# Performance work log

Measured on AMD Instinct MI355X. Metric: run time of the kernel, lower is better.

The kernel has to match this reference:

```python
import jax, jax.numpy as jnp
import numpy as np

N, E, ND, ED, NG = 100000, 1600000, 256, 32, 64
H1, H2 = 5, 1  # hard-coded hidden widths in the module
EPS = 1e-5


def setup_inputs() -> dict:
    key = jax.random.key(0)
    ks = jax.random.split(key, 32)

    def rn(k, shape, scale=0.05):
        return jax.random.normal(k, shape, dtype=jnp.float32) * scale

    inp = {
        "x": rn(ks[0], (N, ND), 1.0),
        "edge_attr": rn(ks[1], (E, ED), 1.0),
        "edge_index": jax.random.randint(ks[2], (2, E), 0, N, dtype=jnp.int32),
        "batch_idx": jnp.sort(jax.random.randint(ks[3], (N,), 0, NG, dtype=jnp.int32)),
        # conv1: ResGatedGraphConv(ND -> H1) with edge_dim=ED, root_weight, bias
        "Wk1": rn(ks[4], (ND, H1)), "bk1": jnp.zeros((H1,), jnp.float32),
        "Wq1": rn(ks[5], (ND, H1)), "bq1": jnp.zeros((H1,), jnp.float32),
        "Wv1": rn(ks[6], (ND, H1)), "bv1": jnp.zeros((H1,), jnp.float32),
        "We1": rn(ks[7], (ED, H1)), "be1": jnp.zeros((H1,), jnp.float32),
        "Ws1": rn(ks[8], (ND, H1)), "b1": jnp.zeros((H1,), jnp.float32),
        # GraphNorm(H1): weight=1, bias=0, mean_scale=1 at init
        "gw": jnp.ones((H1,), jnp.float32), "gb": jnp.zeros((H1,), jnp.float32),
        "gms": jnp.ones((H1,), jnp.float32),
        # conv2: ResGatedGraphConv(H1 -> H2)
        "Wk2": rn(ks[9], (H1, H2)), "bk2": jnp.zeros((H2,), jnp.float32),
        "Wq2": rn(ks[10], (H1, H2)), "bq2": jnp.zeros((H2,), jnp.float32),
        "Wv2": rn(ks[11], (H1, H2)), "bv2": jnp.zeros((H2,), jnp.float32),
        "We2": rn(ks[12], (ED, H2)), "be2": jnp.zeros((H2,), jnp.float32),
        "Ws2": rn(ks[13], (H1, H2)), "b2": jnp.zeros((H2,), jnp.float32),
    }
    return inp


def _res_gated_conv(x, src, dst, eatt, Wk, bk, Wq, bq, Wv, bv, We, be, Ws, b):
    # PyG ResGatedGraphConv: msg = sigmoid(k_i + q_j) * v_j with edge_attr
    # projection added to k, q, v; aggr='add'; plus root skip and bias.
    k = x @ Wk + bk            # [N,H]
    q = x @ Wq + bq            # [N,H]
    v = x @ Wv + bv            # [N,H]
    e = eatt @ We + be         # [E,H]
    gate = jax.nn.sigmoid(k[dst] + q[src] + 2.0 * e)  # (k_i+e)+(q_j+e)
    msg = gate * (v[src] + e)                          # [E,H]
    agg = jax.ops.segment_sum(msg, dst, num_segments=x.shape[0])
    return agg + x @ Ws + b


def _graph_norm(x, batch, w, b, ms):
    ones = jnp.ones((x.shape[0], 1), x.dtype)
    cnt = jnp.maximum(jax.ops.segment_sum(ones, batch, num_segments=NG), 1.0)
    mean = jax.ops.segment_sum(x, batch, num_segments=NG) / cnt
    out = x - mean[batch] * ms
    var = jax.ops.segment_sum(out * out, batch, num_segments=NG) / cnt
    inv_std = jax.lax.rsqrt(var + EPS)
    return w * out * inv_std[batch] + b


def reference(x, edge_attr, edge_index, batch_idx,
              Wk1, bk1, Wq1, bq1, Wv1, bv1, We1, be1, Ws1, b1,
              gw, gb, gms,
              Wk2, bk2, Wq2, bq2, Wv2, bv2, We2, be2, Ws2, b2):
    src, dst = edge_index[0], edge_index[1]
    h = _res_gated_conv(x, src, dst, edge_attr, Wk1, bk1, Wq1, bq1, Wv1, bv1,
                        We1, be1, Ws1, b1)
    h = _graph_norm(h, batch_idx, gw, gb, gms)
    h = jax.nn.relu(h)
    h = _res_gated_conv(h, src, dst, edge_attr, Wk2, bk2, Wq2, bq2, Wv2, bv2,
                        We2, be2, Ws2, b2)
    return jax.nn.sigmoid(h)
```

## Files before the change

kernel.cpp:

```cpp
#include <hip/hip_runtime.h>
#include <math.h>

#define ND 256
#define ED 32
#define H1 5
#define NG 64
#define SCAN_TILE 1024

__device__ __forceinline__ float sigf(float z) {
    return 1.0f / (1.0f + __expf(-z));
}

__global__ void node_proj1(const float* __restrict__ x,
                           const float* __restrict__ Wk, const float* __restrict__ bk,
                           const float* __restrict__ Wq, const float* __restrict__ bq,
                           const float* __restrict__ Wv, const float* __restrict__ bv,
                           const float* __restrict__ Ws, const float* __restrict__ br,
                           float* __restrict__ kqv, float* __restrict__ h, int N)
{
    int n = blockIdx.x * blockDim.x + threadIdx.x;
    if (n >= N) return;

    float acc[20];
#pragma unroll
    for (int c = 0; c < H1; c++) {
        acc[c]      = bk[c];
        acc[5 + c]  = bq[c];
        acc[10 + c] = bv[c];
        acc[15 + c] = br[c];
    }

    const float4* X4 = (const float4*)(x + (size_t)n * ND);
#pragma unroll 2
    for (int j4 = 0; j4 < ND / 4; j4++) {
        float4 xv = X4[j4];
        float xr[4] = {xv.x, xv.y, xv.z, xv.w};
#pragma unroll
        for (int r = 0; r < 4; r++) {
            int j = j4 * 4 + r;
#pragma unroll
            for (int c = 0; c < H1; c++) {
                acc[c]      += xr[r] * Wk[j * H1 + c];
                acc[5 + c]  += xr[r] * Wq[j * H1 + c];
                acc[10 + c] += xr[r] * Wv[j * H1 + c];
                acc[15 + c] += xr[r] * Ws[j * H1 + c];
            }
        }
    }

    float* row = kqv + (size_t)n * 16;
#pragma unroll
    for (int c = 0; c < H1; c++) {
        row[c]      = acc[5 + c];
        row[5 + c]  = acc[10 + c];
        row[10 + c] = acc[c];
    }
    row[15] = 0.0f;
#pragma unroll
    for (int c = 0; c < H1; c++) h[(size_t)n * H1 + c] = acc[15 + c];
}

__global__ void hist_dst(const int* __restrict__ ei, int* __restrict__ cnt, int E)
{
    int e = blockIdx.x * blockDim.x + threadIdx.x;
    if (e < E) atomicAdd(&cnt[ei[E + e]], 1);
}

__global__ void scan_part(const int* __restrict__ cnt, int* __restrict__ bsum, int N)
{
    int t = threadIdx.x;
    int base = blockIdx.x * SCAN_TILE + t * 4;
    int s = 0;
    if (base + 3 < N) {
        int4 v = *(const int4*)(cnt + base);
        s = v.x + v.y + v.z + v.w;
    } else {
        for (int i = 0; i < 4; i++) if (base + i < N) s += cnt[base + i];
    }
#pragma unroll
    for (int off = 32; off >= 1; off >>= 1) s += __shfl_xor(s, off);
    __shared__ int wsum[4];
    if ((t & 63) == 0) wsum[t >> 6] = s;
    __syncthreads();
    if (t == 0) bsum[blockIdx.x] = wsum[0] + wsum[1] + wsum[2] + wsum[3];
}

__global__ void scan_blocksums(int* __restrict__ bsum, int nb)
{
    __shared__ int a[1024], b[1024];
    int t = threadIdx.x;
    int v = (t < nb) ? bsum[t] : 0;
    a[t] = v;
    __syncthreads();
    int* in = a; int* out = b;
    for (int off = 1; off < 1024; off <<= 1) {
        out[t] = in[t] + ((t >= off) ? in[t - off] : 0);
        __syncthreads();
        int* tmp = in; in = out; out = tmp;
    }
    if (t < nb) bsum[t] = in[t] - v;
}

__global__ void scan_final(const int* __restrict__ cnt, const int* __restrict__ bsum,
                           int* __restrict__ offs, int* __restrict__ cursor, int N, int E)
{
    int t = threadIdx.x;
    int lane = t & 63;
    int wave = t >> 6;
    int base = blockIdx.x * SCAN_TILE + t * 4;

    int v0 = 0, v1 = 0, v2 = 0, v3 = 0;
    if (base + 3 < N) {
        int4 v = *(const int4*)(cnt + base);
        v0 = v.x; v1 = v.y; v2 = v.z; v3 = v.w;
    } else {
        if (base + 0 < N) v0 = cnt[base + 0];
        if (base + 1 < N) v1 = cnt[base + 1];
        if (base + 2 < N) v2 = cnt[base + 2];
        if (base + 3 < N) v3 = cnt[base + 3];
    }
    int s = v0 + v1 + v2 + v3;

    int inc = s;
#pragma unroll
    for (int off = 1; off < 64; off <<= 1) {
        int u = __shfl_up(inc, off);
        if (lane >= off) inc += u;
    }

    __shared__ int wtot[4];
    if (lane == 63) wtot[wave] = inc;
    __syncthreads();
    int woff = 0;
#pragma unroll
    for (int w = 0; w < 4; w++) woff += (w < wave) ? wtot[w] : 0;

    int excl = bsum[blockIdx.x] + woff + (inc - s);

    if (base < N) {
        int p0 = excl, p1 = p0 + v0, p2 = p1 + v1, p3 = p2 + v2;
        if (base + 3 < N) {
            *(int4*)(offs + base)   = make_int4(p0, p1, p2, p3);
            *(int4*)(cursor + base) = make_int4(p0, p1, p2, p3);
        } else {
            if (base + 0 < N) { offs[base + 0] = p0; cursor[base + 0] = p0; }
            if (base + 1 < N) { offs[base + 1] = p1; cursor[base + 1] = p1; }
            if (base + 2 < N) { offs[base + 2] = p2; cursor[base + 2] = p2; }
            if (base + 3 < N) { offs[base + 3] = p3; cursor[base + 3] = p3; }
        }
    }
    if (blockIdx.x == 0 && t == 0) offs[N] = E;
}

__global__ void edge_scatter(const float* __restrict__ ea, const int* __restrict__ ei,
                             const float* __restrict__ We1, const float* __restrict__ be1,
                             const float* __restrict__ We2, const float* __restrict__ be2,
                             int* __restrict__ cursor, float* __restrict__ sorted, int E)
{
    __shared__ float lds[256 * 33];
    int t = threadIdx.x;
    int base = blockIdx.x * 256;
    int nEdge = min(256, E - base);

    const float4* g = (const float4*)(ea + (size_t)base * ED);
    for (int k = t; k < nEdge * 8; k += 256) {
        float4 v = g[k];
        int f = k * 4;
        int r = f >> 5, c = f & 31;
        float* p = &lds[r * 33 + c];
        p[0] = v.x; p[1] = v.y; p[2] = v.z; p[3] = v.w;
    }
    __syncthreads();

    int e = base + t;
    if (e >= E) return;

    float acc0 = be1[0], acc1 = be1[1], acc2 = be1[2], acc3 = be1[3], acc4 = be1[4];
    float acc5 = be2[0];
    const float* myrow = &lds[t * 33];
#pragma unroll
    for (int j = 0; j < ED; j++) {
        float a = myrow[j];
        acc0 += a * We1[j * H1 + 0];
        acc1 += a * We1[j * H1 + 1];
        acc2 += a * We1[j * H1 + 2];
        acc3 += a * We1[j * H1 + 3];
        acc4 += a * We1[j * H1 + 4];
        acc5 += a * We2[j];
    }

    int s = ei[e];
    int d = ei[E + e];
    int pos = atomicAdd(&cursor[d], 1);

    float4* rec = (float4*)(sorted + (size_t)pos * 8);
    rec[0] = make_float4(__int_as_float(s), acc0, acc1, acc2);
    rec[1] = make_float4(acc3, acc4, acc5, 0.0f);
}

__global__ void aggregate1(const float* __restrict__ sorted, const int* __restrict__ offs,
                           const float* __restrict__ kqv, float* __restrict__ h, int N)
{
    int t = threadIdx.x;
    int n = blockIdx.x * 16 + (t >> 4);
    int lane = t & 15;
    if (n >= N) return;

    int start = offs[n], end = offs[n + 1];

    const float4* row = (const float4*)(kqv + (size_t)n * 16);
    float4 kA = row[2];
    float4 kB = row[3];
    float kd0 = kA.z, kd1 = kA.w, kd2 = kB.x, kd3 = kB.y, kd4 = kB.z;

    float m0 = 0, m1 = 0, m2 = 0, m3 = 0, m4 = 0;
    for (int i = start + lane; i < end; i += 16) {
        const float4* rec = (const float4*)(sorted + (size_t)i * 8);
        float4 r0 = rec[0];
        float4 r1 = rec[1];
        int s = __float_as_int(r0.x);
        const float4* srow = (const float4*)(kqv + (size_t)s * 16);
        float4 q0 = srow[0];
        float4 q1 = srow[1];
        float4 q2 = srow[2];
        m0 += sigf(kd0 + q0.x + 2.0f * r0.y) * (q1.y + r0.y);
        m1 += sigf(kd1 + q0.y + 2.0f * r0.z) * (q1.z + r0.z);
        m2 += sigf(kd2 + q0.z + 2.0f * r0.w) * (q1.w + r0.w);
        m3 += sigf(kd3 + q0.w + 2.0f * r1.x) * (q2.x + r1.x);
        m4 += sigf(kd4 + q1.x + 2.0f * r1.y) * (q2.y + r1.y);
    }

#pragma unroll
    for (int off = 8; off >= 1; off >>= 1) {
        m0 += __shfl_xor(m0, off);
        m1 += __shfl_xor(m1, off);
        m2 += __shfl_xor(m2, off);
        m3 += __shfl_xor(m3, off);
        m4 += __shfl_xor(m4, off);
    }

    if (lane == 0) {
        size_t base = (size_t)n * H1;
        h[base + 0] += m0;
        h[base + 1] += m1;
        h[base + 2] += m2;
        h[base + 3] += m3;
        h[base + 4] += m4;
    }
}

__global__ void norm_reduce(const float* __restrict__ h, const int* __restrict__ B,
                            const float* __restrict__ gw, const float* __restrict__ gb,
                            const float* __restrict__ gms,
                            float* __restrict__ scale, float* __restrict__ shift, int N)
{
    int g = blockIdx.x;

    int lo = 0, hi = N;
    while (lo < hi) { int mid = (lo + hi) >> 1; if (B[mid] < g) lo = mid + 1; else hi = mid; }
    int start = lo;
    hi = N;
    while (lo < hi) { int mid = (lo + hi) >> 1; if (B[mid] < g + 1) lo = mid + 1; else hi = mid; }
    int end = lo;

    float sum[H1] = {0, 0, 0, 0, 0};
    float sq[H1]  = {0, 0, 0, 0, 0};
    for (int i = start + threadIdx.x; i < end; i += blockDim.x) {
#pragma unroll
        for (int c = 0; c < H1; c++) {
            float v = h[(size_t)i * H1 + c];
            sum[c] += v;
            sq[c]  += v * v;
        }
    }

#pragma unroll
    for (int off = 32; off >= 1; off >>= 1) {
#pragma unroll
        for (int c = 0; c < H1; c++) {
            sum[c] += __shfl_xor(sum[c], off);
            sq[c]  += __shfl_xor(sq[c], off);
        }
    }

    __shared__ float ls[4][2 * H1];
    int wave = threadIdx.x >> 6;
    int lane = threadIdx.x & 63;
    if (lane == 0) {
#pragma unroll
        for (int c = 0; c < H1; c++) { ls[wave][c] = sum[c]; ls[wave][H1 + c] = sq[c]; }
    }
    __syncthreads();

    if (threadIdx.x == 0) {
        float cnt = fmaxf((float)(end - start), 1.0f);
#pragma unroll
        for (int c = 0; c < H1; c++) {
            float s0 = ls[0][c] + ls[1][c] + ls[2][c] + ls[3][c];
            float q0 = ls[0][H1 + c] + ls[1][H1 + c] + ls[2][H1 + c] + ls[3][H1 + c];
            float mean = s0 / cnt;
            float ms   = gms[c];
            float var  = q0 / cnt - mean * mean * ms * (2.0f - ms);
            float inv  = rsqrtf(var + 1e-5f);
            float sc   = gw[c] * inv;
            scale[g * H1 + c] = sc;
            shift[g * H1 + c] = gb[c] - sc * mean * ms;
        }
    }
}

__global__ void norm_apply_proj2(const float* __restrict__ h, const int* __restrict__ B,
                                 const float* __restrict__ scale, const float* __restrict__ shift,
                                 const float* __restrict__ Wk2, const float* __restrict__ bk2,
                                 const float* __restrict__ Wq2, const float* __restrict__ bq2,
                                 const float* __restrict__ Wv2, const float* __restrict__ bv2,
                                 const float* __restrict__ Ws2, const float* __restrict__ b2,
                                 float4* __restrict__ kqv2, float* __restrict__ root2, int N)
{
    int n = blockIdx.x * blockDim.x + threadIdx.x;
    if (n >= N) return;

    int g = B[n];
    float k2 = bk2[0], q2 = bq2[0], v2 = bv2[0], s2 = b2[0];
#pragma unroll
    for (int c = 0; c < H1; c++) {
        float hn = scale[g * H1 + c] * h[(size_t)n * H1 + c] + shift[g * H1 + c];
        hn = fmaxf(hn, 0.0f);
        k2 += hn * Wk2[c];
        q2 += hn * Wq2[c];
        v2 += hn * Wv2[c];
        s2 += hn * Ws2[c];
    }
    kqv2[n]  = make_float4(k2, q2, v2, 0.0f);
    root2[n] = s2;
}

__global__ void aggregate2(const float* __restrict__ sorted, const int* __restrict__ offs,
                           const float4* __restrict__ kqv2, const float* __restrict__ root2,
                           float* __restrict__ out, int N)
{
    int t = threadIdx.x;
    int n = blockIdx.x * 16 + (t >> 4);
    int lane = t & 15;
    if (n >= N) return;

    int start = offs[n], end = offs[n + 1];
    float kd = kqv2[n].x;

    float m = 0;
    for (int i = start + lane; i < end; i += 16) {
        const float4* rec = (const float4*)(sorted + (size_t)i * 8);
        float4 r0 = rec[0];
        float4 r1 = rec[1];
        int s = __float_as_int(r0.x);
        float e2 = r1.z;
        float4 sv = kqv2[s];
        m += sigf(kd + sv.y + 2.0f * e2) * (sv.z + e2);
    }

#pragma unroll
    for (int off = 8; off >= 1; off >>= 1) m += __shfl_xor(m, off);

    if (lane == 0) out[n] = sigf(root2[n] + m);
}

extern "C" void kernel_launch(void* const* d_in, const int* in_sizes, int n_in,
                              void* d_out, int out_size, void* d_ws, size_t ws_size,
                              hipStream_t stream)
{
    const float* x   = (const float*)d_in[0];
    const float* ea  = (const float*)d_in[1];
    const int*   ei  = (const int*)d_in[2];
    const int*   B   = (const int*)d_in[3];
    const float* Wk1 = (const float*)d_in[4];
    const float* bk1 = (const float*)d_in[5];
    const float* Wq1 = (const float*)d_in[6];
    const float* bq1 = (const float*)d_in[7];
    const float* Wv1 = (const float*)d_in[8];
    const float* bv1 = (const float*)d_in[9];
    const float* We1 = (const float*)d_in[10];
    const float* be1 = (const float*)d_in[11];
    const float* Ws1 = (const float*)d_in[12];
    const float* b1  = (const float*)d_in[13];
    const float* gw  = (const float*)d_in[14];
    const float* gb  = (const float*)d_in[15];
    const float* gms = (const float*)d_in[16];
    const float* Wk2 = (const float*)d_in[17];
    const float* bk2 = (const float*)d_in[18];
    const float* Wq2 = (const float*)d_in[19];
    const float* bq2 = (const float*)d_in[20];
    const float* Wv2 = (const float*)d_in[21];
    const float* bv2 = (const float*)d_in[22];
    const float* We2 = (const float*)d_in[23];
    const float* be2 = (const float*)d_in[24];
    const float* Ws2 = (const float*)d_in[25];
    const float* b2  = (const float*)d_in[26];

    const int N = in_sizes[0] / ND;
    const int E = in_sizes[1] / ED;
    const int nb = (N + SCAN_TILE - 1) / SCAN_TILE;

    float* ws      = (float*)d_ws;
    float* kqv     = ws;
    float* h       = kqv + (size_t)N * 16;
    float* sorted  = h + (size_t)N * H1;
    int*   cnt     = (int*)(sorted + (size_t)E * 8);
    int*   offs    = cnt + N;
    int*   cursor  = offs + N + 4;
    int*   bsum    = cursor + N;
    float* scale   = (float*)(bsum + 1024);
    float* shift   = scale + NG * H1;
    float* kqv2f   = shift + NG * H1 + 2;
    kqv2f = (float*)(bsum + 1024) + 640;
    float* root2   = kqv2f + (size_t)N * 4;
    float4* kqv2   = (float4*)kqv2f;

    dim3 blk(256);
    dim3 gN((N + 255) / 256);
    dim3 gE((E + 255) / 256);
    dim3 gAgg((N + 15) / 16);

    hipMemsetAsync(cnt, 0, (size_t)N * sizeof(int), stream);

    hist_dst<<<gE, blk, 0, stream>>>(ei, cnt, E);
    node_proj1<<<gN, blk, 0, stream>>>(x, Wk1, bk1, Wq1, bq1, Wv1, bv1, Ws1, b1,
                                       kqv, h, N);
    scan_part<<<nb, 256, 0, stream>>>(cnt, bsum, N);
    scan_blocksums<<<1, 1024, 0, stream>>>(bsum, nb);
    scan_final<<<nb, 256, 0, stream>>>(cnt, bsum, offs, cursor, N, E);
    edge_scatter<<<gE, blk, 0, stream>>>(ea, ei, We1, be1, We2, be2, cursor, sorted, E);
    aggregate1<<<gAgg, blk, 0, stream>>>(sorted, offs, kqv, h, N);
    norm_reduce<<<NG, blk, 0, stream>>>(h, B, gw, gb, gms, scale, shift, N);
    norm_apply_proj2<<<gN, blk, 0, stream>>>(h, B, scale, shift,
                                             Wk2, bk2, Wq2, bq2, Wv2, bv2, Ws2, b2,
                                             kqv2, root2, N);
    aggregate2<<<gAgg, blk, 0, stream>>>(sorted, offs, kqv2, root2, (float*)d_out, N);
}
```

Measured before the change: 652.1 us.

## Project edges in edge order into packed fp16 records and sort only edge ids

Edge projections are now computed in original edge order and fused with the destination histogram. Each edge becomes a 16-byte record holding the src index and six fp16 projections, replacing the 32-byte fp32 record that was written scattered into CSR order. A separate pass scatters only edge ids into CSR order, and the aggregation kernels follow the id into the record array. This cuts scattered write volume and record size, but adds an indirect random gather per edge in both aggregations and loses precision by storing edge projections in fp16.

```diff
diff --git a/kernel.cpp b/kernel.cpp
--- a/kernel.cpp
+++ b/kernel.cpp
@@ -10,6 +10,11 @@
 __device__ __forceinline__ float sigf(float z) {
     return 1.0f / (1.0f + __expf(-z));
 }
+
+union PK {
+    int4 i;
+    struct { int src; _Float16 e[6]; } f;
+};
 
 __global__ void node_proj1(const float* __restrict__ x,
                            const float* __restrict__ Wk, const float* __restrict__ bk,
@@ -60,10 +65,55 @@
     for (int c = 0; c < H1; c++) h[(size_t)n * H1 + c] = acc[15 + c];
 }
 
-__global__ void hist_dst(const int* __restrict__ ei, int* __restrict__ cnt, int E)
-{
-    int e = blockIdx.x * blockDim.x + threadIdx.x;
-    if (e < E) atomicAdd(&cnt[ei[E + e]], 1);
+__global__ void edge_proj_hist(const float* __restrict__ ea, const int* __restrict__ ei,
+                               const float* __restrict__ We1, const float* __restrict__ be1,
+                               const float* __restrict__ We2, const float* __restrict__ be2,
+                               int* __restrict__ cnt, int4* __restrict__ recs, int E)
+{
+    __shared__ float wlds[ED * 6];
+    int t = threadIdx.x;
+    if (t < ED * 6) {
+        int j = t / 6, cc = t % 6;
+        wlds[t] = (cc < 5) ? We1[j * H1 + cc] : We2[j];
+    }
+    __syncthreads();
+
+    int g = t >> 3;
+    int c = t & 7;
+    int e = blockIdx.x * 32 + g;
+    if (e >= E) return;
+
+    float4 a = *(const float4*)(ea + (size_t)e * ED + c * 4);
+    float ar[4] = {a.x, a.y, a.z, a.w};
+
+    float p[6];
+#pragma unroll
+    for (int cc = 0; cc < 6; cc++)
+        p[cc] = (c == 0) ? ((cc < 5) ? be1[cc] : be2[0]) : 0.0f;
+
+#pragma unroll
+    for (int r = 0; r < 4; r++) {
+        int j = c * 4 + r;
+#pragma unroll
+        for (int cc = 0; cc < 6; cc++) p[cc] += ar[r] * wlds[j * 6 + cc];
+    }
+
+#pragma unroll
+    for (int off = 1; off < 8; off <<= 1) {
+#pragma unroll
+        for (int cc = 0; cc < 6; cc++) p[cc] += __shfl_xor(p[cc], off);
+    }
+
+    if (c == 0) {
+        int s = ei[e];
+        int d = ei[E + e];
+        atomicAdd(&cnt[d], 1);
+        PK pk;
+        pk.f.src = s;
+#pragma unroll
+        for (int cc = 0; cc < 6; cc++) pk.f.e[cc] = (_Float16)p[cc];
+        recs[e] = pk.i;
+    }
 }
 
 __global__ void scan_part(const int* __restrict__ cnt, int* __restrict__ bsum, int N)
@@ -152,53 +202,18 @@
     if (blockIdx.x == 0 && t == 0) offs[N] = E;
 }
 
-__global__ void edge_scatter(const float* __restrict__ ea, const int* __restrict__ ei,
-                             const float* __restrict__ We1, const float* __restrict__ be1,
-                             const float* __restrict__ We2, const float* __restrict__ be2,
-                             int* __restrict__ cursor, float* __restrict__ sorted, int E)
-{
-    __shared__ float lds[256 * 33];
-    int t = threadIdx.x;
-    int base = blockIdx.x * 256;
-    int nEdge = min(256, E - base);
-
-    const float4* g = (const float4*)(ea + (size_t)base * ED);
-    for (int k = t; k < nEdge * 8; k += 256) {
-        float4 v = g[k];
-        int f = k * 4;
-        int r = f >> 5, c = f & 31;
-        float* p = &lds[r * 33 + c];
-        p[0] = v.x; p[1] = v.y; p[2] = v.z; p[3] = v.w;
-    }
-    __syncthreads();
-
-    int e = base + t;
+__global__ void scatter_eid(const int* __restrict__ ei, int* __restrict__ cursor,
+                            int* __restrict__ sorted_eid, int E)
+{
+    int e = blockIdx.x * blockDim.x + threadIdx.x;
     if (e >= E) return;
-
-    float acc0 = be1[0], acc1 = be1[1], acc2 = be1[2], acc3 = be1[3], acc4 = be1[4];
-    float acc5 = be2[0];
-    const float* myrow = &lds[t * 33];
-#pragma unroll
-    for (int j = 0; j < ED; j++) {
-        float a = myrow[j];
-        acc0 += a * We1[j * H1 + 0];
-        acc1 += a * We1[j * H1 + 1];
-        acc2 += a * We1[j * H1 + 2];
-        acc3 += a * We1[j * H1 + 3];
-        acc4 += a * We1[j * H1 + 4];
-        acc5 += a * We2[j];
-    }
-
-    int s = ei[e];
     int d = ei[E + e];
     int pos = atomicAdd(&cursor[d], 1);
-
-    float4* rec = (float4*)(sorted + (size_t)pos * 8);
-    rec[0] = make_float4(__int_as_float(s), acc0, acc1, acc2);
-    rec[1] = make_float4(acc3, acc4, acc5, 0.0f);
-}
-
-__global__ void aggregate1(const float* __restrict__ sorted, const int* __restrict__ offs,
+    sorted_eid[pos] = e;
+}
+
+__global__ void aggregate1(const int* __restrict__ sorted_eid, const int4* __restrict__ recs,
+                           const int* __restrict__ offs,
                            const float* __restrict__ kqv, float* __restrict__ h, int N)
 {
     int t = threadIdx.x;
@@ -215,19 +230,20 @@
 
     float m0 = 0, m1 = 0, m2 = 0, m3 = 0, m4 = 0;
     for (int i = start + lane; i < end; i += 16) {
-        const float4* rec = (const float4*)(sorted + (size_t)i * 8);
-        float4 r0 = rec[0];
-        float4 r1 = rec[1];
-        int s = __float_as_int(r0.x);
+        int eid = sorted_eid[i];
+        PK pk; pk.i = recs[eid];
+        int s = pk.f.src;
+        float e0 = (float)pk.f.e[0], e1 = (float)pk.f.e[1], e2 = (float)pk.f.e[2];
+        float e3 = (float)pk.f.e[3], e4 = (float)pk.f.e[4];
         const float4* srow = (const float4*)(kqv + (size_t)s * 16);
         float4 q0 = srow[0];
         float4 q1 = srow[1];
         float4 q2 = srow[2];
-        m0 += sigf(kd0 + q0.x + 2.0f * r0.y) * (q1.y + r0.y);
-        m1 += sigf(kd1 + q0.y + 2.0f * r0.z) * (q1.z + r0.z);
-        m2 += sigf(kd2 + q0.z + 2.0f * r0.w) * (q1.w + r0.w);
-        m3 += sigf(kd3 + q0.w + 2.0f * r1.x) * (q2.x + r1.x);
-        m4 += sigf(kd4 + q1.x + 2.0f * r1.y) * (q2.y + r1.y);
+        m0 += sigf(kd0 + q0.x + 2.0f * e0) * (q1.y + e0);
+        m1 += sigf(kd1 + q0.y + 2.0f * e1) * (q1.z + e1);
+        m2 += sigf(kd2 + q0.z + 2.0f * e2) * (q1.w + e2);
+        m3 += sigf(kd3 + q0.w + 2.0f * e3) * (q2.x + e3);
+        m4 += sigf(kd4 + q1.x + 2.0f * e4) * (q2.y + e4);
     }
 
 #pragma unroll
@@ -335,7 +351,8 @@
     root2[n] = s2;
 }
 
-__global__ void aggregate2(const float* __restrict__ sorted, const int* __restrict__ offs,
+__global__ void aggregate2(const int* __restrict__ sorted_eid, const int4* __restrict__ recs,
+                           const int* __restrict__ offs,
                            const float4* __restrict__ kqv2, const float* __restrict__ root2,
                            float* __restrict__ out, int N)
 {
@@ -349,11 +366,10 @@
 
     float m = 0;
     for (int i = start + lane; i < end; i += 16) {
-        const float4* rec = (const float4*)(sorted + (size_t)i * 8);
-        float4 r0 = rec[0];
-        float4 r1 = rec[1];
-        int s = __float_as_int(r0.x);
-        float e2 = r1.z;
+        int eid = sorted_eid[i];
+        PK pk; pk.i = recs[eid];
+        int s = pk.f.src;
+        float e2 = (float)pk.f.e[5];
         float4 sv = kqv2[s];
         m += sigf(kd + sv.y + 2.0f * e2) * (sv.z + e2);
     }
@@ -400,39 +416,40 @@
     const int E = in_sizes[1] / ED;
     const int nb = (N + SCAN_TILE - 1) / SCAN_TILE;
 
-    float* ws      = (float*)d_ws;
-    float* kqv     = ws;
-    float* h       = kqv + (size_t)N * 16;
-    float* sorted  = h + (size_t)N * H1;
-    int*   cnt     = (int*)(sorted + (size_t)E * 8);
-    int*   offs    = cnt + N;
-    int*   cursor  = offs + N + 4;
-    int*   bsum    = cursor + N;
-    float* scale   = (float*)(bsum + 1024);
-    float* shift   = scale + NG * H1;
-    float* kqv2f   = shift + NG * H1 + 2;
-    kqv2f = (float*)(bsum + 1024) + 640;
-    float* root2   = kqv2f + (size_t)N * 4;
-    float4* kqv2   = (float4*)kqv2f;
+    float* ws         = (float*)d_ws;
+    float* kqv        = ws;
+    float* h          = kqv + (size_t)N * 16;
+    int4*  recs       = (int4*)(h + (size_t)N * H1);
+    int*   sorted_eid = (int*)(recs + (size_t)E);
+    int*   cnt        = sorted_eid + E;
+    int*   offs       = cnt + N;
+    int*   cursor     = offs + N + 4;
+    int*   bsum       = cursor + N;
+    float* scale      = (float*)(bsum + 1024);
+    float* shift      = scale + NG * H1;
+    float* kqv2f      = shift + NG * H1;
+    float* root2      = kqv2f + (size_t)N * 4;
+    float4* kqv2      = (float4*)kqv2f;
 
     dim3 blk(256);
     dim3 gN((N + 255) / 256);
     dim3 gE((E + 255) / 256);
+    dim3 gE8((E + 31) / 32);
     dim3 gAgg((N + 15) / 16);
 
     hipMemsetAsync(cnt, 0, (size_t)N * sizeof(int), stream);
 
-    hist_dst<<<gE, blk, 0, stream>>>(ei, cnt, E);
     node_proj1<<<gN, blk, 0, stream>>>(x, Wk1, bk1, Wq1, bq1, Wv1, bv1, Ws1, b1,
                                        kqv, h, N);
+    edge_proj_hist<<<gE8, blk, 0, stream>>>(ea, ei, We1, be1, We2, be2, cnt, recs, E);
     scan_part<<<nb, 256, 0, stream>>>(cnt, bsum, N);
     scan_blocksums<<<1, 1024, 0, stream>>>(bsum, nb);
     scan_final<<<nb, 256, 0, stream>>>(cnt, bsum, offs, cursor, N, E);
-    edge_scatter<<<gE, blk, 0, stream>>>(ea, ei, We1, be1, We2, be2, cursor, sorted, E);
-    aggregate1<<<gAgg, blk, 0, stream>>>(sorted, offs, kqv, h, N);
+    scatter_eid<<<gE, blk, 0, stream>>>(ei, cursor, sorted_eid, E);
+    aggregate1<<<gAgg, blk, 0, stream>>>(sorted_eid, recs, offs, kqv, h, N);
     norm_reduce<<<NG, blk, 0, stream>>>(h, B, gw, gb, gms, scale, shift, N);
     norm_apply_proj2<<<gN, blk, 0, stream>>>(h, B, scale, shift,
                                              Wk2, bk2, Wq2, bq2, Wv2, bv2, Ws2, b2,
                                              kqv2, root2, N);
-    aggregate2<<<gAgg, blk, 0, stream>>>(sorted, offs, kqv2, root2, (float*)d_out, N);
-}
+    aggregate2<<<gAgg, blk, 0, stream>>>(sorted_eid, recs, offs, kqv2, root2, (float*)d_out, N);
+}
```

Measured after the change: 718.0 us. 1.1x slower.
